# Optimization experiments

Hardware: AMD Instinct MI355X
Metric: run time of the kernel (lower is better)

Reference implementation:

```python
import jax, jax.numpy as jnp
import numpy as np

EMBED = 1024
HEADS = 16
HEAD_DIM = EMBED // HEADS
B, T = 2, 2048
ROPE_THETA = 10000.0


def _rope(x):
    # x: [B, H, T, D]; standard half-split rotary embedding, applied per head
    D = x.shape[-1]
    inv_freq = 1.0 / (ROPE_THETA ** (jnp.arange(0, D, 2, dtype=jnp.float32) / D))  # [D/2]
    freqs = jnp.arange(x.shape[2], dtype=jnp.float32)[:, None] * inv_freq[None, :]  # [T, D/2]
    cos = jnp.cos(freqs).astype(x.dtype)  # [T, D/2]
    sin = jnp.sin(freqs).astype(x.dtype)
    x1, x2 = x[..., : D // 2], x[..., D // 2 :]
    return jnp.concatenate([x1 * cos - x2 * sin, x2 * cos + x1 * sin], axis=-1)


def setup_inputs() -> dict:
    key = jax.random.key(0)
    ks = jax.random.split(key, 5)
    s = 1.0 / np.sqrt(EMBED)
    return {
        "x": jax.random.normal(ks[0], (B, T, EMBED), dtype=jnp.float32),
        "Wq": jax.random.normal(ks[1], (EMBED, EMBED), dtype=jnp.float32) * s,
        "bq": jnp.zeros((EMBED,), dtype=jnp.float32),
        "Wk": jax.random.normal(ks[2], (EMBED, EMBED), dtype=jnp.float32) * s,
        "bk": jnp.zeros((EMBED,), dtype=jnp.float32),
        "Wv": jax.random.normal(ks[3], (EMBED, EMBED), dtype=jnp.float32) * s,
        "bv": jnp.zeros((EMBED,), dtype=jnp.float32),
        "Wo": jax.random.normal(ks[4], (EMBED, EMBED), dtype=jnp.float32) * s,
        "bo": jnp.zeros((EMBED,), dtype=jnp.float32),
    }


def reference(x, Wq, bq, Wk, bk, Wv, bv, Wo, bo):
    Bb, Tt, C = x.shape
    H, D = HEADS, HEAD_DIM
    # torch Linear: y = x @ W.T + b
    def proj(W, b):
        return (jnp.einsum("btc,oc->bto", x, W) + b).reshape(Bb, Tt, H, D).transpose(0, 2, 1, 3)

    q = _rope(proj(Wq, bq))  # [B, H, T, D]
    k = _rope(proj(Wk, bk))
    v = proj(Wv, bv)
    scale = jnp.sqrt(jnp.asarray(D, dtype=x.dtype))
    scores = jnp.einsum("bhtd,bhsd->bhts", q, k) / scale  # [B, H, T, T]
    attn = jax.nn.softmax(scores, axis=-1)  # dropout = identity in eval mode
    out = jnp.einsum("bhts,bhsd->bhtd", attn, v)  # [B, H, T, D]
    out = out.transpose(0, 2, 1, 3).reshape(Bb, Tt, C)
    return jnp.einsum("btc,oc->bto", out, Wo) + bo
```

## Files before the change

### kernel.cpp

```cpp
#include <hip/hip_runtime.h>
#include <hip/hip_bf16.h>

#define EMBED 1024
#define HEADS 16
#define HDIM 64
#define BATCH 2
#define SEQ 2048
#define MTOT (BATCH*SEQ)

typedef __attribute__((ext_vector_type(2))) float f32x2;
typedef __attribute__((ext_vector_type(4))) float f32x4;
typedef __attribute__((ext_vector_type(16))) float f32x16;
typedef __attribute__((ext_vector_type(4))) short s16x4;
typedef __attribute__((ext_vector_type(8))) short bf16x8;
typedef __attribute__((ext_vector_type(4))) int i32x4;

static __device__ __forceinline__ short f2bf(float f) {
  unsigned u = __builtin_bit_cast(unsigned, f);
  unsigned r = (u + 0x7fffu + ((u >> 16) & 1u)) >> 16;
  return (short)r;
}
static __device__ __forceinline__ float bf2f(short s) {
  unsigned u = ((unsigned)(unsigned short)s) << 16;
  return __builtin_bit_cast(float, u);
}
static __device__ __forceinline__ int pack2bf_fast(float lo, float hi) {
  unsigned ulo = __builtin_bit_cast(unsigned, lo) + 0x8000u;
  unsigned uhi = __builtin_bit_cast(unsigned, hi) + 0x8000u;
  int r;
  asm("v_cvt_pk_bf16_f32 %0, %1, %2" : "=v"(r)
      : "v"(__builtin_bit_cast(float, ulo)), "v"(__builtin_bit_cast(float, uhi)));
  return r;
}
static __device__ __forceinline__ void pswap(int &a, int &b) {
  asm("v_permlane32_swap_b32 %0, %1" : "+v"(a), "+v"(b));
}

typedef __attribute__((address_space(1))) const void gvoid_t;
typedef __attribute__((address_space(3))) void lvoid_t;
static __device__ __forceinline__ void gload_lds16(const void* g, void* l) {
  __builtin_amdgcn_global_load_lds((gvoid_t*)g, (lvoid_t*)l, 16, 0, 0);
}

__global__ __launch_bounds__(256) void cvt_bf16(
    const float* __restrict__ x,
    const float* __restrict__ Wq, const float* __restrict__ Wk,
    const float* __restrict__ Wv, const float* __restrict__ Wo,
    short* __restrict__ xb,
    short* __restrict__ Wqb, short* __restrict__ Wkb,
    short* __restrict__ Wvb, short* __restrict__ Wob,
    f32x2* __restrict__ tab)
{
  int i = blockIdx.x * 256 + threadIdx.x;
  if (i >= 2097152) {
    int i2 = i - 2097152;
    int t = i2 >> 5, j = i2 & 31;
    float invf = exp2f(-(float)j * 0.4152410118609203f);
    float sn, cs;
    sincosf((float)t * invf, &sn, &cs);
    f32x2 e; e[0] = cs; e[1] = sn;
    tab[i2] = e;
    return;
  }
  const float* src; short* dst; int off;
  if (i < 1048576) { src = x; dst = xb; off = i; }
  else {
    int j = i - 1048576;
    int w = j >> 18; off = j & 262143;
    src = (w == 0) ? Wq : (w == 1) ? Wk : (w == 2) ? Wv : Wo;
    dst = (w == 0) ? Wqb : (w == 1) ? Wkb : (w == 2) ? Wvb : Wob;
  }
  f32x4 v = ((const f32x4*)src)[off];
  s16x4 h;
#pragma unroll
  for (int j = 0; j < 4; ++j) h[j] = f2bf(v[j]);
  ((s16x4*)dst)[off] = h;
}

__global__ __launch_bounds__(256) void qkv_gemm(
    const short* __restrict__ xb,
    const short* __restrict__ Wqb, const short* __restrict__ Wkb, const short* __restrict__ Wvb,
    const float* __restrict__ bq, const float* __restrict__ bk, const float* __restrict__ bv,
    const f32x2* __restrict__ tab,
    short* __restrict__ Qb, short* __restrict__ Kb, short* __restrict__ Vb)
{
  __shared__ short As[2][128][64];
  __shared__ short Bs[2][128][64];
  int tid = threadIdx.x;
  int lane = tid & 63, wid = tid >> 6;
  int wm = wid >> 1, wn = wid & 1;
  int bm = blockIdx.x / 24;
  int bncol = blockIdx.x % 24;
  int wsel = bncol >> 3, bnn = bncol & 7;
  const short* W    = (wsel == 0) ? Wqb : (wsel == 1) ? Wkb : Wvb;
  const float* bias = (wsel == 0) ? bq : (wsel == 1) ? bk : bv;

  f32x4 acc[4][4] = {};

  const short* Abase = xb + (size_t)bm * 128 * EMBED;
  const short* Bbase = W + (size_t)bnn * 128 * EMBED;
  char* AsB = (char*)&As[0][0][0];
  char* BsB = (char*)&Bs[0][0][0];
  const int TSZ = 128 * 64 * 2;

#pragma unroll
  for (int i = 0; i < 4; ++i) {
    int s = tid + i * 256;
    int row = s >> 3, c = s & 7;
    int cs = c ^ (row & 7);
    gload_lds16(&Abase[(size_t)row * EMBED + cs * 8],
                AsB + i * 4096 + wid * 1024 + lane * 16);
    gload_lds16(&Bbase[(size_t)row * EMBED + cs * 8],
                BsB + i * 4096 + wid * 1024 + lane * 16);
  }
  __syncthreads();

  for (int kt = 0; kt < EMBED / 64; ++kt) {
    int cur = kt & 1;
    if (kt + 1 < EMBED / 64) {
#pragma unroll
      for (int i = 0; i < 4; ++i) {
        int s = tid + i * 256;
        int row = s >> 3, c = s & 7;
        int cs = c ^ (row & 7);
        gload_lds16(&Abase[(size_t)row * EMBED + (kt + 1) * 64 + cs * 8],
                    AsB + (cur ^ 1) * TSZ + i * 4096 + wid * 1024 + lane * 16);
        gload_lds16(&Bbase[(size_t)row * EMBED + (kt + 1) * 64 + cs * 8],
                    BsB + (cur ^ 1) * TSZ + i * 4096 + wid * 1024 + lane * 16);
      }
    }

#pragma unroll
    for (int kk = 0; kk < 2; ++kk) {
      int cp = ((kk * 4 + (lane >> 4)) ^ (lane & 7)) * 8;
      bf16x8 af[4], bfr[4];
#pragma unroll
      for (int mf = 0; mf < 4; ++mf)
        af[mf] = *(const bf16x8*)&As[cur][wm * 64 + mf * 16 + (lane & 15)][cp];
#pragma unroll
      for (int nf = 0; nf < 4; ++nf)
        bfr[nf] = *(const bf16x8*)&Bs[cur][wn * 64 + nf * 16 + (lane & 15)][cp];
      if (wsel == 2) {
#pragma unroll
        for (int mf = 0; mf < 4; ++mf)
#pragma unroll
          for (int nf = 0; nf < 4; ++nf)
            acc[mf][nf] = __builtin_amdgcn_mfma_f32_16x16x32_bf16(bfr[mf], af[nf], acc[mf][nf], 0, 0, 0);
      } else {
#pragma unroll
        for (int mf = 0; mf < 4; ++mf)
#pragma unroll
          for (int nf = 0; nf < 4; ++nf)
            acc[mf][nf] = __builtin_amdgcn_mfma_f32_16x16x32_bf16(af[mf], bfr[nf], acc[mf][nf], 0, 0, 0);
      }
    }
    __syncthreads();
  }

  if (wsel < 2) {
    short* dst = (wsel == 0) ? Qb : Kb;
    float sc = (wsel == 0) ? 0.18033688011112042f : 1.0f;
#pragma unroll
    for (int nf = 0; nf < 2; ++nf) {
      int col = bnn * 128 + wn * 64 + nf * 16 + (lane & 15);
      int h = col >> 6, j = col & 31;
      float b1 = bias[col], b2 = bias[col + 32];
#pragma unroll
      for (int mf = 0; mf < 4; ++mf) {
        int row0 = bm * 128 + wm * 64 + mf * 16 + ((lane >> 4) << 2);
#pragma unroll
        for (int r = 0; r < 4; ++r) {
          int m = row0 + r;
          int b_ = m >> 11, t = m & (SEQ - 1);
          f32x2 e = tab[t * 32 + j];
          float a1 = acc[mf][nf][r] + b1;
          float a2 = acc[mf][nf + 2][r] + b2;
          size_t o = (((size_t)(b_ * HEADS + h)) * SEQ + t) * HDIM + j;
          dst[o]      = f2bf((a1 * e[0] - a2 * e[1]) * sc);
          dst[o + 32] = f2bf((a2 * e[0] + a1 * e[1]) * sc);
        }
      }
    }
  } else {
#pragma unroll
    for (int mf = 0; mf < 4; ++mf) {
#pragma unroll
      for (int r = 0; r < 4; ++r) {
        int cch = bnn * 128 + wn * 64 + mf * 16 + ((lane >> 4) << 2) + r;
        int h = cch >> 6, d = cch & 63;
        float bb = bias[cch];
#pragma unroll
        for (int nf = 0; nf < 4; ++nf) {
          int m = bm * 128 + wm * 64 + nf * 16 + (lane & 15);
          int b_ = m >> 11, t = m & (SEQ - 1);
          Vb[((size_t)(b_ * HEADS + h) * HDIM + d) * SEQ + t] = f2bf(acc[mf][nf][r] + bb);
        }
      }
    }
  }
}

#define QBLK 128
#define KBLK 64

__global__ __launch_bounds__(256, 2) void attn_kernel(
    const short* __restrict__ Qb, const short* __restrict__ Kb,
    const short* __restrict__ Vb, short* __restrict__ Ob)
{
  __shared__ short Ks[2][KBLK][68];
  __shared__ short Vs[2][HDIM][68];

  int tid = threadIdx.x, lane = tid & 63, wid = tid >> 6;
  int l31 = lane & 31, lhi = lane >> 5;

  int bid = blockIdx.x;
  int swz = (bid & 7) * 64 + (bid >> 3);
  int qi = swz & 15, bh = swz >> 4;
  int b = bh >> 4, h = bh & 15;

  const short* Qp = Qb + ((size_t)bh * SEQ + qi * QBLK + wid * 32) * HDIM;
  const short* Kp = Kb + (size_t)bh * SEQ * HDIM;
  const short* Vp = Vb + (size_t)bh * HDIM * SEQ;

  bf16x8 qf[4];
#pragma unroll
  for (int cc = 0; cc < 4; ++cc)
    qf[cc] = *(const bf16x8*)&Qp[(size_t)l31 * HDIM + cc * 16 + lhi * 8];

  f32x16 oacc0 = {}, oacc1 = {}, lacc = {};
  bf16x8 vones;
#pragma unroll
  for (int j = 0; j < 8; ++j) vones[j] = (short)0x3F80;

  bf16x8 kreg[2], vreg[2];
#pragma unroll
  for (int i = 0; i < 2; ++i) {
    int s = tid + i * 256;
    kreg[i] = *(const bf16x8*)&Kp[(size_t)(s >> 3) * HDIM + (s & 7) * 8];
    vreg[i] = *(const bf16x8*)&Vp[(size_t)(s >> 3) * SEQ + (s & 7) * 8];
  }
#pragma unroll
  for (int i = 0; i < 2; ++i) {
    int s = tid + i * 256;
    *(bf16x8*)&Ks[0][s >> 3][(s & 7) * 8] = kreg[i];
    *(bf16x8*)&Vs[0][s >> 3][(s & 7) * 8] = vreg[i];
  }
  __syncthreads();

  for (int kt = 0; kt < SEQ / KBLK; ++kt) {
    int cur = kt & 1;
    if (kt + 1 < SEQ / KBLK) {
#pragma unroll
      for (int i = 0; i < 2; ++i) {
        int s = tid + i * 256;
        kreg[i] = *(const bf16x8*)&Kp[(size_t)((kt + 1) * KBLK + (s >> 3)) * HDIM + (s & 7) * 8];
        vreg[i] = *(const bf16x8*)&Vp[(size_t)(s >> 3) * SEQ + (kt + 1) * KBLK + (s & 7) * 8];
      }
    }

    f32x16 s0 = {}, s1 = {};
#pragma unroll
    for (int cc = 0; cc < 4; ++cc) {
      bf16x8 a0 = *(const bf16x8*)&Ks[cur][l31][cc * 16 + lhi * 8];
      bf16x8 a1 = *(const bf16x8*)&Ks[cur][32 + l31][cc * 16 + lhi * 8];
      s0 = __builtin_amdgcn_mfma_f32_32x32x16_bf16(a0, qf[cc], s0, 0, 0, 0);
      s1 = __builtin_amdgcn_mfma_f32_32x32x16_bf16(a1, qf[cc], s1, 0, 0, 0);
    }
    f32x16 p0, p1;
#pragma unroll
    for (int i = 0; i < 16; ++i) {
      p0[i] = __builtin_amdgcn_exp2f(s0[i]);
      p1[i] = __builtin_amdgcn_exp2f(s1[i]);
    }

#pragma unroll
    for (int c = 0; c < 2; ++c) {
      int w0 = pack2bf_fast(p0[8 * c + 0], p0[8 * c + 1]);
      int w1 = pack2bf_fast(p0[8 * c + 2], p0[8 * c + 3]);
      int w2 = pack2bf_fast(p0[8 * c + 4], p0[8 * c + 5]);
      int w3 = pack2bf_fast(p0[8 * c + 6], p0[8 * c + 7]);
      pswap(w0, w2);
      pswap(w1, w3);
      i32x4 pw; pw[0] = w0; pw[1] = w1; pw[2] = w2; pw[3] = w3;
      bf16x8 pa = __builtin_bit_cast(bf16x8, pw);

      bf16x8 vf0 = *(const bf16x8*)&Vs[cur][l31][c * 16 + lhi * 8];
      bf16x8 vf1 = *(const bf16x8*)&Vs[cur][32 + l31][c * 16 + lhi * 8];
      lacc = __builtin_amdgcn_mfma_f32_32x32x16_bf16(pa, vones, lacc, 0, 0, 0);
      oacc0 = __builtin_amdgcn_mfma_f32_32x32x16_bf16(pa, vf0, oacc0, 0, 0, 0);
      oacc1 = __builtin_amdgcn_mfma_f32_32x32x16_bf16(pa, vf1, oacc1, 0, 0, 0);
    }
#pragma unroll
    for (int c = 0; c < 2; ++c) {
      int w0 = pack2bf_fast(p1[8 * c + 0], p1[8 * c + 1]);
      int w1 = pack2bf_fast(p1[8 * c + 2], p1[8 * c + 3]);
      int w2 = pack2bf_fast(p1[8 * c + 4], p1[8 * c + 5]);
      int w3 = pack2bf_fast(p1[8 * c + 6], p1[8 * c + 7]);
      pswap(w0, w2);
      pswap(w1, w3);
      i32x4 pw; pw[0] = w0; pw[1] = w1; pw[2] = w2; pw[3] = w3;
      bf16x8 pa = __builtin_bit_cast(bf16x8, pw);

      bf16x8 vf0 = *(const bf16x8*)&Vs[cur][l31][32 + c * 16 + lhi * 8];
      bf16x8 vf1 = *(const bf16x8*)&Vs[cur][32 + l31][32 + c * 16 + lhi * 8];
      lacc = __builtin_amdgcn_mfma_f32_32x32x16_bf16(pa, vones, lacc, 0, 0, 0);
      oacc0 = __builtin_amdgcn_mfma_f32_32x32x16_bf16(pa, vf0, oacc0, 0, 0, 0);
      oacc1 = __builtin_amdgcn_mfma_f32_32x32x16_bf16(pa, vf1, oacc1, 0, 0, 0);
    }

    if (kt + 1 < SEQ / KBLK) {
#pragma unroll
      for (int i = 0; i < 2; ++i) {
        int s = tid + i * 256;
        *(bf16x8*)&Ks[cur ^ 1][s >> 3][(s & 7) * 8] = kreg[i];
        *(bf16x8*)&Vs[cur ^ 1][s >> 3][(s & 7) * 8] = vreg[i];
      }
      __syncthreads();
    }
  }

#pragma unroll
  for (int r = 0; r < 16; ++r) {
    int qrow = (r & 3) + 8 * (r >> 2) + 4 * lhi;
    int t = qi * QBLK + wid * 32 + qrow;
    float inv = 1.0f / lacc[r];
    size_t base = ((size_t)(b * SEQ + t)) * EMBED + h * HDIM;
    Ob[base + l31]      = f2bf(oacc0[r] * inv);
    Ob[base + 32 + l31] = f2bf(oacc1[r] * inv);
  }
}

__global__ __launch_bounds__(256) void out_gemm(
    const short* __restrict__ A, const short* __restrict__ Wob,
    const float* __restrict__ bo, float* __restrict__ C)
{
  __shared__ short As[2][64][64];
  __shared__ short Bs[2][128][64];
  int tid = threadIdx.x;
  int lane = tid & 63, wid = tid >> 6;
  int bm = blockIdx.x >> 3, bn = blockIdx.x & 7;

  f32x4 acc[8] = {};
  const short* Abase = A + (size_t)bm * 64 * EMBED;
  const short* Bbase = Wob + (size_t)bn * 128 * EMBED;
  char* AsB = (char*)&As[0][0][0];
  char* BsB = (char*)&Bs[0][0][0];
  const int ATSZ = 64 * 64 * 2;
  const int BTSZ = 128 * 64 * 2;

#pragma unroll
  for (int i = 0; i < 2; ++i) {
    int s = tid + i * 256;
    int row = s >> 3, c = s & 7;
    int cs = c ^ (row & 7);
    gload_lds16(&Abase[(size_t)row * EMBED + cs * 8],
                AsB + i * 4096 + wid * 1024 + lane * 16);
  }
#pragma unroll
  for (int i = 0; i < 4; ++i) {
    int s = tid + i * 256;
    int row = s >> 3, c = s & 7;
    int cs = c ^ (row & 7);
    gload_lds16(&Bbase[(size_t)row * EMBED + cs * 8],
                BsB + i * 4096 + wid * 1024 + lane * 16);
  }
  __syncthreads();

  for (int kt = 0; kt < EMBED / 64; ++kt) {
    int cur = kt & 1;
    if (kt + 1 < EMBED / 64) {
#pragma unroll
      for (int i = 0; i < 2; ++i) {
        int s = tid + i * 256;
        int row = s >> 3, c = s & 7;
        int cs = c ^ (row & 7);
        gload_lds16(&Abase[(size_t)row * EMBED + (kt + 1) * 64 + cs * 8],
                    AsB + (cur ^ 1) * ATSZ + i * 4096 + wid * 1024 + lane * 16);
      }
#pragma unroll
      for (int i = 0; i < 4; ++i) {
        int s = tid + i * 256;
        int row = s >> 3, c = s & 7;
        int cs = c ^ (row & 7);
        gload_lds16(&Bbase[(size_t)row * EMBED + (kt + 1) * 64 + cs * 8],
                    BsB + (cur ^ 1) * BTSZ + i * 4096 + wid * 1024 + lane * 16);
      }
    }

#pragma unroll
    for (int kk = 0; kk < 2; ++kk) {
      int cp = ((kk * 4 + (lane >> 4)) ^ (lane & 7)) * 8;
      bf16x8 af = *(const bf16x8*)&As[cur][wid * 16 + (lane & 15)][cp];
#pragma unroll
      for (int nf = 0; nf < 8; ++nf) {
        bf16x8 bfr = *(const bf16x8*)&Bs[cur][nf * 16 + (lane & 15)][cp];
        acc[nf] = __builtin_amdgcn_mfma_f32_16x16x32_bf16(af, bfr, acc[nf], 0, 0, 0);
      }
    }
    __syncthreads();
  }

#pragma unroll
  for (int nf = 0; nf < 8; ++nf) {
    int col = bn * 128 + nf * 16 + (lane & 15);
    float bb = bo[col];
    int row0 = bm * 64 + wid * 16 + ((lane >> 4) << 2);
#pragma unroll
    for (int r = 0; r < 4; ++r)
      C[(size_t)(row0 + r) * EMBED + col] = acc[nf][r] + bb;
  }
}

extern "C" void kernel_launch(void* const* d_in, const int* in_sizes, int n_in,
                              void* d_out, int out_size, void* d_ws, size_t ws_size,
                              hipStream_t stream) {
  const float* x  = (const float*)d_in[0];
  const float* Wq = (const float*)d_in[1];
  const float* bq = (const float*)d_in[2];
  const float* Wk = (const float*)d_in[3];
  const float* bk = (const float*)d_in[4];
  const float* Wv = (const float*)d_in[5];
  const float* bv = (const float*)d_in[6];
  const float* Wo = (const float*)d_in[7];
  const float* bo = (const float*)d_in[8];
  float* out = (float*)d_out;
  char* ws = (char*)d_ws;

  const size_t MB = 1u << 20;
  short* Qb  = (short*)(ws);
  short* Kb  = (short*)(ws + 8 * MB);
  short* Vb  = (short*)(ws + 16 * MB);
  short* XOb = (short*)(ws + 24 * MB);
  short* Wqb = (short*)(ws + 32 * MB);
  short* Wkb = (short*)(ws + 34 * MB);
  short* Wvb = (short*)(ws + 36 * MB);
  short* Wob = (short*)(ws + 38 * MB);
  f32x2* tab = (f32x2*)(ws + 40 * MB);

  cvt_bf16<<<dim3(8448), dim3(256), 0, stream>>>(x, Wq, Wk, Wv, Wo, XOb, Wqb, Wkb, Wvb, Wob, tab);
  qkv_gemm<<<dim3(32 * 24), dim3(256), 0, stream>>>(XOb, Wqb, Wkb, Wvb, bq, bk, bv, tab, Qb, Kb, Vb);
  attn_kernel<<<dim3(BATCH * HEADS * (SEQ / QBLK)), dim3(256), 0, stream>>>(Qb, Kb, Vb, XOb);
  out_gemm<<<dim3(64 * 8), dim3(256), 0, stream>>>(XOb, Wob, bo, out);
}
```

Baseline: 117.8 us.

## Shrink attention query block to 64 with 16x16 MFMA and staged output stores

The attention kernel now gives each block 64 queries instead of 128, with 16 query rows per wave. It switches from 32x32 to 16x16x32 MFMA tiles, which removes the permlane swaps, and raises launch bounds to 4 blocks per CU so more blocks run and more are resident. Output is staged through LDS so it can be written to global memory as 16-byte vector stores. The QKV GEMM also drops LDS double buffering in favor of a simple load-sync-compute loop, which shrinks LDS use but exposes load latency. Smaller query tiles mean each K/V tile is reused across fewer queries, so K/V traffic doubles.

```diff
diff --git a/kernel.cpp b/kernel.cpp
--- a/kernel.cpp
+++ b/kernel.cpp
@@ -31,9 +31,6 @@
   asm("v_cvt_pk_bf16_f32 %0, %1, %2" : "=v"(r)
       : "v"(__builtin_bit_cast(float, ulo)), "v"(__builtin_bit_cast(float, uhi)));
   return r;
-}
-static __device__ __forceinline__ void pswap(int &a, int &b) {
-  asm("v_permlane32_swap_b32 %0, %1" : "+v"(a), "+v"(b));
 }
 
 typedef __attribute__((address_space(1))) const void gvoid_t;
@@ -84,8 +81,8 @@
     const f32x2* __restrict__ tab,
     short* __restrict__ Qb, short* __restrict__ Kb, short* __restrict__ Vb)
 {
-  __shared__ short As[2][128][64];
-  __shared__ short Bs[2][128][64];
+  __shared__ short As[128][64];
+  __shared__ short Bs[128][64];
   int tid = threadIdx.x;
   int lane = tid & 63, wid = tid >> 6;
   int wm = wid >> 1, wn = wid & 1;
@@ -99,47 +96,31 @@
 
   const short* Abase = xb + (size_t)bm * 128 * EMBED;
   const short* Bbase = W + (size_t)bnn * 128 * EMBED;
-  char* AsB = (char*)&As[0][0][0];
-  char* BsB = (char*)&Bs[0][0][0];
-  const int TSZ = 128 * 64 * 2;
-
-#pragma unroll
-  for (int i = 0; i < 4; ++i) {
-    int s = tid + i * 256;
-    int row = s >> 3, c = s & 7;
-    int cs = c ^ (row & 7);
-    gload_lds16(&Abase[(size_t)row * EMBED + cs * 8],
-                AsB + i * 4096 + wid * 1024 + lane * 16);
-    gload_lds16(&Bbase[(size_t)row * EMBED + cs * 8],
-                BsB + i * 4096 + wid * 1024 + lane * 16);
-  }
-  __syncthreads();
+  char* AsB = (char*)&As[0][0];
+  char* BsB = (char*)&Bs[0][0];
 
   for (int kt = 0; kt < EMBED / 64; ++kt) {
-    int cur = kt & 1;
-    if (kt + 1 < EMBED / 64) {
-#pragma unroll
-      for (int i = 0; i < 4; ++i) {
-        int s = tid + i * 256;
-        int row = s >> 3, c = s & 7;
-        int cs = c ^ (row & 7);
-        gload_lds16(&Abase[(size_t)row * EMBED + (kt + 1) * 64 + cs * 8],
-                    AsB + (cur ^ 1) * TSZ + i * 4096 + wid * 1024 + lane * 16);
-        gload_lds16(&Bbase[(size_t)row * EMBED + (kt + 1) * 64 + cs * 8],
-                    BsB + (cur ^ 1) * TSZ + i * 4096 + wid * 1024 + lane * 16);
-      }
-    }
-
+#pragma unroll
+    for (int i = 0; i < 4; ++i) {
+      int s = tid + i * 256;
+      int row = s >> 3, c = s & 7;
+      int cs = c ^ (row & 7);
+      gload_lds16(&Abase[(size_t)row * EMBED + kt * 64 + cs * 8],
+                  AsB + i * 4096 + wid * 1024 + lane * 16);
+      gload_lds16(&Bbase[(size_t)row * EMBED + kt * 64 + cs * 8],
+                  BsB + i * 4096 + wid * 1024 + lane * 16);
+    }
+    __syncthreads();
 #pragma unroll
     for (int kk = 0; kk < 2; ++kk) {
       int cp = ((kk * 4 + (lane >> 4)) ^ (lane & 7)) * 8;
       bf16x8 af[4], bfr[4];
 #pragma unroll
       for (int mf = 0; mf < 4; ++mf)
-        af[mf] = *(const bf16x8*)&As[cur][wm * 64 + mf * 16 + (lane & 15)][cp];
+        af[mf] = *(const bf16x8*)&As[wm * 64 + mf * 16 + (lane & 15)][cp];
 #pragma unroll
       for (int nf = 0; nf < 4; ++nf)
-        bfr[nf] = *(const bf16x8*)&Bs[cur][wn * 64 + nf * 16 + (lane & 15)][cp];
+        bfr[nf] = *(const bf16x8*)&Bs[wn * 64 + nf * 16 + (lane & 15)][cp];
       if (wsel == 2) {
 #pragma unroll
         for (int mf = 0; mf < 4; ++mf)
@@ -200,10 +181,10 @@
   }
 }
 
-#define QBLK 128
+#define QBLK 64
 #define KBLK 64
 
-__global__ __launch_bounds__(256, 2) void attn_kernel(
+__global__ __launch_bounds__(256, 4) void attn_kernel(
     const short* __restrict__ Qb, const short* __restrict__ Kb,
     const short* __restrict__ Vb, short* __restrict__ Ob)
 {
@@ -211,26 +192,29 @@
   __shared__ short Vs[2][HDIM][68];
 
   int tid = threadIdx.x, lane = tid & 63, wid = tid >> 6;
-  int l31 = lane & 31, lhi = lane >> 5;
+  int l15 = lane & 15, lg = lane >> 4;
 
   int bid = blockIdx.x;
-  int swz = (bid & 7) * 64 + (bid >> 3);
-  int qi = swz & 15, bh = swz >> 4;
+  int swz = (bid & 7) * 128 + (bid >> 3);
+  int qi = swz & 31, bh = swz >> 5;
   int b = bh >> 4, h = bh & 15;
 
-  const short* Qp = Qb + ((size_t)bh * SEQ + qi * QBLK + wid * 32) * HDIM;
+  const short* Qp = Qb + ((size_t)bh * SEQ + qi * QBLK + wid * 16) * HDIM;
   const short* Kp = Kb + (size_t)bh * SEQ * HDIM;
   const short* Vp = Vb + (size_t)bh * HDIM * SEQ;
 
-  bf16x8 qf[4];
-#pragma unroll
-  for (int cc = 0; cc < 4; ++cc)
-    qf[cc] = *(const bf16x8*)&Qp[(size_t)l31 * HDIM + cc * 16 + lhi * 8];
-
-  f32x16 oacc0 = {}, oacc1 = {}, lacc = {};
+  bf16x8 qf[2];
+#pragma unroll
+  for (int ec = 0; ec < 2; ++ec)
+    qf[ec] = *(const bf16x8*)&Qp[(size_t)l15 * HDIM + ec * 32 + lg * 8];
+
+  f32x4 oacc[4] = {};
+  f32x4 lacc = {};
   bf16x8 vones;
 #pragma unroll
   for (int j = 0; j < 8; ++j) vones[j] = (short)0x3F80;
+
+  int arow = 8 * (l15 >> 2) + (l15 & 3);
 
   bf16x8 kreg[2], vreg[2];
 #pragma unroll
@@ -258,54 +242,35 @@
       }
     }
 
-    f32x16 s0 = {}, s1 = {};
-#pragma unroll
-    for (int cc = 0; cc < 4; ++cc) {
-      bf16x8 a0 = *(const bf16x8*)&Ks[cur][l31][cc * 16 + lhi * 8];
-      bf16x8 a1 = *(const bf16x8*)&Ks[cur][32 + l31][cc * 16 + lhi * 8];
-      s0 = __builtin_amdgcn_mfma_f32_32x32x16_bf16(a0, qf[cc], s0, 0, 0, 0);
-      s1 = __builtin_amdgcn_mfma_f32_32x32x16_bf16(a1, qf[cc], s1, 0, 0, 0);
-    }
-    f32x16 p0, p1;
-#pragma unroll
-    for (int i = 0; i < 16; ++i) {
-      p0[i] = __builtin_amdgcn_exp2f(s0[i]);
-      p1[i] = __builtin_amdgcn_exp2f(s1[i]);
-    }
-
-#pragma unroll
-    for (int c = 0; c < 2; ++c) {
-      int w0 = pack2bf_fast(p0[8 * c + 0], p0[8 * c + 1]);
-      int w1 = pack2bf_fast(p0[8 * c + 2], p0[8 * c + 3]);
-      int w2 = pack2bf_fast(p0[8 * c + 4], p0[8 * c + 5]);
-      int w3 = pack2bf_fast(p0[8 * c + 6], p0[8 * c + 7]);
-      pswap(w0, w2);
-      pswap(w1, w3);
-      i32x4 pw; pw[0] = w0; pw[1] = w1; pw[2] = w2; pw[3] = w3;
+#pragma unroll
+    for (int kc = 0; kc < 2; ++kc) {
+      f32x4 s0 = {}, s1 = {};
+#pragma unroll
+      for (int ec = 0; ec < 2; ++ec) {
+        bf16x8 a0 = *(const bf16x8*)&Ks[cur][kc * 32 + 0 + arow][ec * 32 + lg * 8];
+        bf16x8 a1 = *(const bf16x8*)&Ks[cur][kc * 32 + 4 + arow][ec * 32 + lg * 8];
+        s0 = __builtin_amdgcn_mfma_f32_16x16x32_bf16(a0, qf[ec], s0, 0, 0, 0);
+        s1 = __builtin_amdgcn_mfma_f32_16x16x32_bf16(a1, qf[ec], s1, 0, 0, 0);
+      }
+      float p0[4], p1[4];
+#pragma unroll
+      for (int r = 0; r < 4; ++r) {
+        p0[r] = __builtin_amdgcn_exp2f(s0[r]);
+        p1[r] = __builtin_amdgcn_exp2f(s1[r]);
+      }
+      i32x4 pw;
+      pw[0] = pack2bf_fast(p0[0], p0[1]);
+      pw[1] = pack2bf_fast(p0[2], p0[3]);
+      pw[2] = pack2bf_fast(p1[0], p1[1]);
+      pw[3] = pack2bf_fast(p1[2], p1[3]);
       bf16x8 pa = __builtin_bit_cast(bf16x8, pw);
 
-      bf16x8 vf0 = *(const bf16x8*)&Vs[cur][l31][c * 16 + lhi * 8];
-      bf16x8 vf1 = *(const bf16x8*)&Vs[cur][32 + l31][c * 16 + lhi * 8];
-      lacc = __builtin_amdgcn_mfma_f32_32x32x16_bf16(pa, vones, lacc, 0, 0, 0);
-      oacc0 = __builtin_amdgcn_mfma_f32_32x32x16_bf16(pa, vf0, oacc0, 0, 0, 0);
-      oacc1 = __builtin_amdgcn_mfma_f32_32x32x16_bf16(pa, vf1, oacc1, 0, 0, 0);
-    }
-#pragma unroll
-    for (int c = 0; c < 2; ++c) {
-      int w0 = pack2bf_fast(p1[8 * c + 0], p1[8 * c + 1]);
-      int w1 = pack2bf_fast(p1[8 * c + 2], p1[8 * c + 3]);
-      int w2 = pack2bf_fast(p1[8 * c + 4], p1[8 * c + 5]);
-      int w3 = pack2bf_fast(p1[8 * c + 6], p1[8 * c + 7]);
-      pswap(w0, w2);
-      pswap(w1, w3);
-      i32x4 pw; pw[0] = w0; pw[1] = w1; pw[2] = w2; pw[3] = w3;
-      bf16x8 pa = __builtin_bit_cast(bf16x8, pw);
-
-      bf16x8 vf0 = *(const bf16x8*)&Vs[cur][l31][32 + c * 16 + lhi * 8];
-      bf16x8 vf1 = *(const bf16x8*)&Vs[cur][32 + l31][32 + c * 16 + lhi * 8];
-      lacc = __builtin_amdgcn_mfma_f32_32x32x16_bf16(pa, vones, lacc, 0, 0, 0);
-      oacc0 = __builtin_amdgcn_mfma_f32_32x32x16_bf16(pa, vf0, oacc0, 0, 0, 0);
-      oacc1 = __builtin_amdgcn_mfma_f32_32x32x16_bf16(pa, vf1, oacc1, 0, 0, 0);
+#pragma unroll
+      for (int df = 0; df < 4; ++df) {
+        bf16x8 vf = *(const bf16x8*)&Vs[cur][df * 16 + l15][kc * 32 + lg * 8];
+        oacc[df] = __builtin_amdgcn_mfma_f32_16x16x32_bf16(vf, pa, oacc[df], 0, 0, 0);
+      }
+      lacc = __builtin_amdgcn_mfma_f32_16x16x32_bf16(vones, pa, lacc, 0, 0, 0);
     }
 
     if (kt + 1 < SEQ / KBLK) {
@@ -319,14 +284,24 @@
     }
   }
 
-#pragma unroll
-  for (int r = 0; r < 16; ++r) {
-    int qrow = (r & 3) + 8 * (r >> 2) + 4 * lhi;
-    int t = qi * QBLK + wid * 32 + qrow;
-    float inv = 1.0f / lacc[r];
-    size_t base = ((size_t)(b * SEQ + t)) * EMBED + h * HDIM;
-    Ob[base + l31]      = f2bf(oacc0[r] * inv);
-    Ob[base + 32 + l31] = f2bf(oacc1[r] * inv);
+  __syncthreads();
+  short (*Os)[68] = (short(*)[68])&Ks[0][0][0];
+  float inv = 1.0f / lacc[0];
+  int qrow = wid * 16 + l15;
+#pragma unroll
+  for (int df = 0; df < 4; ++df) {
+    int d0 = df * 16 + 4 * lg;
+    *(int*)&Os[qrow][d0]     = pack2bf_fast(oacc[df][0] * inv, oacc[df][1] * inv);
+    *(int*)&Os[qrow][d0 + 2] = pack2bf_fast(oacc[df][2] * inv, oacc[df][3] * inv);
+  }
+  __syncthreads();
+#pragma unroll
+  for (int i = 0; i < 2; ++i) {
+    int s = tid + i * 256;
+    int qr = s >> 3, c8 = (s & 7) * 8;
+    int t = qi * QBLK + qr;
+    bf16x8 v = *(const bf16x8*)&Os[qr][c8];
+    *(bf16x8*)&Ob[((size_t)(b * SEQ + t)) * EMBED + h * HDIM + c8] = v;
   }
 }
 
```

Measured after the change: 134.7 us. 14.3% more time.
